# Optimization experiments

Measured on AMD Instinct MI355X. Metric: run time of the kernel, lower is better.

## Reference

```python
import jax, jax.numpy as jnp
import numpy as np


def _sine_theta(v1, v2):
    # v1, v2: [..., 2] edge direction vectors
    cross = v1[..., 0] * v2[..., 1] - v1[..., 1] * v2[..., 0]
    k = jnp.linalg.norm(v1, axis=-1) * jnp.linalg.norm(v2, axis=-1)
    return cross / k


def setup_inputs() -> dict:
    key = jax.random.key(0)
    P, N = 16384, 1024  # P polygons, N points each (N % 4 == 0)
    x_list = jax.random.normal(key, (P, N, 2), dtype=jnp.float32)
    return {"x_list": x_list, "scale": 1}


def reference(x_list, scale):
    # x_list: [P, N, 2] stacked polygons (equivalent to the original python list
    # when all polygons have the same point count N).
    P, N, _ = x_list.shape
    segn = N // 4
    # close the polygon and form consecutive edge vectors v[k] = x[k+1] - x[k]
    xc = jnp.concatenate([x_list, x_list[:, :1]], axis=1)  # [P, N+1, 2]
    v = xc[:, 1:] - xc[:, :-1]                             # [P, N, 2]
    idx = jnp.arange(segn) * 3
    v1 = v[:, idx]       # edge i*3
    v2 = v[:, idx + 1]   # edge i*3+1
    v3 = v[:, idx + 2]   # edge i*3+2
    s12 = _sine_theta(v1, v2)   # [P, segn]
    sina = _sine_theta(v1, v3)  # [P, segn]
    direct = (s12 >= 0).astype(x_list.dtype)
    term = direct * jax.nn.relu(-sina) + (1.0 - direct) * jax.nn.relu(sina)
    seg_loss = term.sum(axis=1) / segn  # [P]
    return (seg_loss * scale).mean()
```

## Files before the change

kernel.cpp:

```cpp
#include <hip/hip_runtime.h>


#define N_PTS     1024
#define SEGN      (N_PTS / 4)
#define BLOCK     256
#define ROW_F4    385

__global__ __launch_bounds__(BLOCK)
void xing_partial_kernel(const float* __restrict__ x,
                         float*       __restrict__ partial)
{
    const int p = blockIdx.x;
    const int t = threadIdx.x;

    __shared__ float rowf[ROW_F4 * 4];

    const float4* src = reinterpret_cast<const float4*>(x + (size_t)p * (N_PTS * 2));
    float4* dst = reinterpret_cast<float4*>(rowf);
    dst[t] = src[t];
    if (t < ROW_F4 - BLOCK) dst[BLOCK + t] = src[BLOCK + t];
    __syncthreads();

    const float2* pts = reinterpret_cast<const float2*>(rowf);
    const float2 a = pts[3 * t + 0];
    const float2 b = pts[3 * t + 1];
    const float2 c = pts[3 * t + 2];
    const float2 d = pts[3 * t + 3];

    const float v1x = b.x - a.x, v1y = b.y - a.y;
    const float v2x = c.x - b.x, v2y = c.y - b.y;
    const float v3x = d.x - c.x, v3y = d.y - c.y;

    const float cross12 = v1x * v2y - v1y * v2x;
    const float cross13 = v1x * v3y - v1y * v3x;

    const float n1 = v1x * v1x + v1y * v1y;
    const float n3 = v3x * v3x + v3y * v3y;
    const float sina = cross13 * rsqrtf(n1 * n3);

    float term = (cross12 >= 0.0f) ? fmaxf(-sina, 0.0f) : fmaxf(sina, 0.0f);

    #pragma unroll
    for (int off = 32; off > 0; off >>= 1)
        term += __shfl_down(term, off, 64);

    __shared__ float wsum[BLOCK / 64];
    const int lane = t & 63;
    const int wid  = t >> 6;
    if (lane == 0) wsum[wid] = term;
    __syncthreads();

    if (t == 0) {
        partial[p] = (wsum[0] + wsum[1]) + (wsum[2] + wsum[3]);
    }
}

__global__ __launch_bounds__(BLOCK)
void xing_reduce_kernel(const float* __restrict__ partial,
                        const int*   __restrict__ scale_p,
                        float*       __restrict__ out,
                        int P)
{
    const int t = threadIdx.x;
    const float4* pf4 = reinterpret_cast<const float4*>(partial);
    const int nf4 = P / 4;

    float sum = 0.0f;
    for (int i = t; i < nf4; i += BLOCK) {
        float4 v = pf4[i];
        sum += (v.x + v.y) + (v.z + v.w);
    }

    #pragma unroll
    for (int off = 32; off > 0; off >>= 1)
        sum += __shfl_down(sum, off, 64);

    __shared__ float wsum[BLOCK / 64];
    const int lane = t & 63;
    const int wid  = t >> 6;
    if (lane == 0) wsum[wid] = sum;
    __syncthreads();

    if (t == 0) {
        const float total = (wsum[0] + wsum[1]) + (wsum[2] + wsum[3]);
        out[0] = total * (float)(*scale_p) / ((float)SEGN * (float)P);
    }
}

extern "C" void kernel_launch(void* const* d_in, const int* in_sizes, int n_in,
                              void* d_out, int out_size, void* d_ws, size_t ws_size,
                              hipStream_t stream)
{
    const float* x       = (const float*)d_in[0];
    const int*   scale_p = (const int*)d_in[1];
    float*       out     = (float*)d_out;
    float*       partial = (float*)d_ws;

    const int P = in_sizes[0] / (N_PTS * 2);

    xing_partial_kernel<<<P, BLOCK, 0, stream>>>(x, partial);
    xing_reduce_kernel<<<1, BLOCK, 0, stream>>>(partial, scale_p, out, P);
}
```

Measured before the change: 182.5 us.

## Process eight polygons per block with double-buffered async global-to-LDS loads

Each block now handles eight polygons instead of one. It stages the next polygon's points straight into shared memory with the AMD global_load_lds builtin while computing on the current buffer, and accumulates per-thread terms across rows before a single block reduction. This is meant to hide load latency and cut per-block launch and reduction overhead. The trade-offs are fewer blocks, which means less memory-level parallelism across the grid, and reliance on the barrier correctly waiting for the async LDS loads to finish.

```diff
diff --git a/kernel.cpp b/kernel.cpp
--- a/kernel.cpp
+++ b/kernel.cpp
@@ -4,66 +4,88 @@
 #define N_PTS     1024
 #define SEGN      (N_PTS / 4)
 #define BLOCK     256
+#define ROWS      8
 #define ROW_F4    385
+#define ROW_FLT   (ROW_F4 * 4)
 
-__global__ __launch_bounds__(BLOCK)
+#define GLOAD_LDS16(g, l)                                                  \
+    __builtin_amdgcn_global_load_lds(                                      \
+        (const __attribute__((address_space(1))) unsigned int*)(g),        \
+        (__attribute__((address_space(3))) unsigned int*)(l), 16, 0, 0)
+
+__device__ __forceinline__ void stage_row(const float* __restrict__ rowsrc,
+                                          float* lbuf, int t)
+{
+    GLOAD_LDS16(rowsrc + 4 * t, lbuf + 4 * t);
+    if (t < ROW_F4 - BLOCK)
+        GLOAD_LDS16(rowsrc + 4 * (BLOCK + t), lbuf + 4 * (BLOCK + t));
+}
+
+__global__ __launch_bounds__(BLOCK, 8)
 void xing_partial_kernel(const float* __restrict__ x,
                          float*       __restrict__ partial)
 {
-    const int p = blockIdx.x;
     const int t = threadIdx.x;
+    const int b = blockIdx.x;
 
-    __shared__ float rowf[ROW_F4 * 4];
+    __shared__ float rowf[2][ROW_FLT];
 
-    const float4* src = reinterpret_cast<const float4*>(x + (size_t)p * (N_PTS * 2));
-    float4* dst = reinterpret_cast<float4*>(rowf);
-    dst[t] = src[t];
-    if (t < ROW_F4 - BLOCK) dst[BLOCK + t] = src[BLOCK + t];
-    __syncthreads();
+    const size_t row0 = (size_t)b * ROWS;
+    stage_row(x + row0 * (N_PTS * 2), rowf[0], t);
 
-    const float2* pts = reinterpret_cast<const float2*>(rowf);
-    const float2 a = pts[3 * t + 0];
-    const float2 b = pts[3 * t + 1];
-    const float2 c = pts[3 * t + 2];
-    const float2 d = pts[3 * t + 3];
+    float acc = 0.0f;
 
-    const float v1x = b.x - a.x, v1y = b.y - a.y;
-    const float v2x = c.x - b.x, v2y = c.y - b.y;
-    const float v3x = d.x - c.x, v3y = d.y - c.y;
+    #pragma unroll
+    for (int r = 0; r < ROWS; ++r) {
+        __syncthreads();
 
-    const float cross12 = v1x * v2y - v1y * v2x;
-    const float cross13 = v1x * v3y - v1y * v3x;
+        if (r + 1 < ROWS)
+            stage_row(x + (row0 + r + 1) * (size_t)(N_PTS * 2),
+                      rowf[(r + 1) & 1], t);
 
-    const float n1 = v1x * v1x + v1y * v1y;
-    const float n3 = v3x * v3x + v3y * v3y;
-    const float sina = cross13 * rsqrtf(n1 * n3);
+        const float2* pts = reinterpret_cast<const float2*>(rowf[r & 1]);
+        const float2 a = pts[3 * t + 0];
+        const float2 bb = pts[3 * t + 1];
+        const float2 c = pts[3 * t + 2];
+        const float2 d = pts[3 * t + 3];
 
-    float term = (cross12 >= 0.0f) ? fmaxf(-sina, 0.0f) : fmaxf(sina, 0.0f);
+        const float v1x = bb.x - a.x,  v1y = bb.y - a.y;
+        const float v2x = c.x - bb.x,  v2y = c.y - bb.y;
+        const float v3x = d.x - c.x,   v3y = d.y - c.y;
+
+        const float cross12 = v1x * v2y - v1y * v2x;
+        const float cross13 = v1x * v3y - v1y * v3x;
+
+        const float n1 = v1x * v1x + v1y * v1y;
+        const float n3 = v3x * v3x + v3y * v3y;
+        const float sina = cross13 * rsqrtf(n1 * n3);
+
+        acc += (cross12 >= 0.0f) ? fmaxf(-sina, 0.0f) : fmaxf(sina, 0.0f);
+    }
 
     #pragma unroll
     for (int off = 32; off > 0; off >>= 1)
-        term += __shfl_down(term, off, 64);
+        acc += __shfl_down(acc, off, 64);
 
     __shared__ float wsum[BLOCK / 64];
     const int lane = t & 63;
     const int wid  = t >> 6;
-    if (lane == 0) wsum[wid] = term;
+    if (lane == 0) wsum[wid] = acc;
     __syncthreads();
 
-    if (t == 0) {
-        partial[p] = (wsum[0] + wsum[1]) + (wsum[2] + wsum[3]);
-    }
+    if (t == 0)
+        partial[b] = (wsum[0] + wsum[1]) + (wsum[2] + wsum[3]);
 }
 
 __global__ __launch_bounds__(BLOCK)
 void xing_reduce_kernel(const float* __restrict__ partial,
                         const int*   __restrict__ scale_p,
                         float*       __restrict__ out,
-                        int P)
+                        int nblk, int P)
 {
     const int t = threadIdx.x;
     const float4* pf4 = reinterpret_cast<const float4*>(partial);
-    const int nf4 = P / 4;
+    const int nf4 = nblk / 4;
 
     float sum = 0.0f;
     for (int i = t; i < nf4; i += BLOCK) {
@@ -96,8 +118,9 @@
     float*       out     = (float*)d_out;
     float*       partial = (float*)d_ws;
 
-    const int P = in_sizes[0] / (N_PTS * 2);
+    const int P    = in_sizes[0] / (N_PTS * 2);
+    const int nblk = P / ROWS;
 
-    xing_partial_kernel<<<P, BLOCK, 0, stream>>>(x, partial);
-    xing_reduce_kernel<<<1, BLOCK, 0, stream>>>(partial, scale_p, out, P);
+    xing_partial_kernel<<<nblk, BLOCK, 0, stream>>>(x, partial);
+    xing_reduce_kernel<<<1, BLOCK, 0, stream>>>(partial, scale_p, out, nblk, P);
 }
```

Measured after the change: 184.6 us. Within noise of the previous version (+1.1%).

## Replace per-polygon blocks with grid-stride persistent loop over segments

Applied to the files above, without the earlier changes.

The partial kernel now launches a fixed grid of 2048 blocks that stride over all segments, reading points straight from global memory instead of staging each polygon row in shared memory. Each thread accumulates many segment terms before the wave reduction, so there are far fewer partial sums for the final kernel. This removes the per-block LDS copy and barrier and is meant to raise memory-level parallelism through the unrolled loop. The trade-off is uncached-looking strided float2 loads, which rely on cache for the overlapping neighbor points.

```diff
diff --git a/kernel.cpp b/kernel.cpp
--- a/kernel.cpp
+++ b/kernel.cpp
@@ -1,69 +1,72 @@
 #include <hip/hip_runtime.h>
 
 
-#define N_PTS     1024
-#define SEGN      (N_PTS / 4)
-#define BLOCK     256
-#define ROW_F4    385
+#define N_PTS 1024
+#define SEGN  (N_PTS / 4)
+#define BLOCK 256
+#define GRID  2048
 
 __global__ __launch_bounds__(BLOCK)
 void xing_partial_kernel(const float* __restrict__ x,
-                         float*       __restrict__ partial)
+                         float*       __restrict__ partial,
+                         int total_segs)
 {
-    const int p = blockIdx.x;
-    const int t = threadIdx.x;
+    const int t   = threadIdx.x;
+    const int tid = blockIdx.x * BLOCK + t;
+    const int gsz = gridDim.x * BLOCK;
 
-    __shared__ float rowf[ROW_F4 * 4];
+    const float2* __restrict__ pts = reinterpret_cast<const float2*>(x);
 
-    const float4* src = reinterpret_cast<const float4*>(x + (size_t)p * (N_PTS * 2));
-    float4* dst = reinterpret_cast<float4*>(rowf);
-    dst[t] = src[t];
-    if (t < ROW_F4 - BLOCK) dst[BLOCK + t] = src[BLOCK + t];
-    __syncthreads();
+    float acc = 0.0f;
 
-    const float2* pts = reinterpret_cast<const float2*>(rowf);
-    const float2 a = pts[3 * t + 0];
-    const float2 b = pts[3 * t + 1];
-    const float2 c = pts[3 * t + 2];
-    const float2 d = pts[3 * t + 3];
+    #pragma unroll 4
+    for (int g = tid; g < total_segs; g += gsz) {
+        const int p = g >> 8;
+        const int s = g & (SEGN - 1);
+        const float2* bp = pts + (p * (N_PTS) + 3 * s);
 
-    const float v1x = b.x - a.x, v1y = b.y - a.y;
-    const float v2x = c.x - b.x, v2y = c.y - b.y;
-    const float v3x = d.x - c.x, v3y = d.y - c.y;
+        const float2 a = bp[0];
+        const float2 b = bp[1];
+        const float2 c = bp[2];
+        const float2 d = bp[3];
 
-    const float cross12 = v1x * v2y - v1y * v2x;
-    const float cross13 = v1x * v3y - v1y * v3x;
+        const float v1x = b.x - a.x, v1y = b.y - a.y;
+        const float v2x = c.x - b.x, v2y = c.y - b.y;
+        const float v3x = d.x - c.x, v3y = d.y - c.y;
 
-    const float n1 = v1x * v1x + v1y * v1y;
-    const float n3 = v3x * v3x + v3y * v3y;
-    const float sina = cross13 * rsqrtf(n1 * n3);
+        const float cross12 = v1x * v2y - v1y * v2x;
+        const float cross13 = v1x * v3y - v1y * v3x;
 
-    float term = (cross12 >= 0.0f) ? fmaxf(-sina, 0.0f) : fmaxf(sina, 0.0f);
+        const float n1 = v1x * v1x + v1y * v1y;
+        const float n3 = v3x * v3x + v3y * v3y;
+        const float sina = cross13 * rsqrtf(n1 * n3);
+
+        acc += (cross12 >= 0.0f) ? fmaxf(-sina, 0.0f) : fmaxf(sina, 0.0f);
+    }
 
     #pragma unroll
     for (int off = 32; off > 0; off >>= 1)
-        term += __shfl_down(term, off, 64);
+        acc += __shfl_down(acc, off, 64);
 
     __shared__ float wsum[BLOCK / 64];
     const int lane = t & 63;
     const int wid  = t >> 6;
-    if (lane == 0) wsum[wid] = term;
+    if (lane == 0) wsum[wid] = acc;
     __syncthreads();
 
-    if (t == 0) {
-        partial[p] = (wsum[0] + wsum[1]) + (wsum[2] + wsum[3]);
-    }
+    if (t == 0)
+        partial[blockIdx.x] = (wsum[0] + wsum[1]) + (wsum[2] + wsum[3]);
 }
 
 __global__ __launch_bounds__(BLOCK)
 void xing_reduce_kernel(const float* __restrict__ partial,
                         const int*   __restrict__ scale_p,
                         float*       __restrict__ out,
-                        int P)
+                        int nblk, int P)
 {
     const int t = threadIdx.x;
     const float4* pf4 = reinterpret_cast<const float4*>(partial);
-    const int nf4 = P / 4;
+    const int nf4 = nblk / 4;
 
     float sum = 0.0f;
     for (int i = t; i < nf4; i += BLOCK) {
@@ -97,7 +100,8 @@
     float*       partial = (float*)d_ws;
 
     const int P = in_sizes[0] / (N_PTS * 2);
+    const int total_segs = P * SEGN;
 
-    xing_partial_kernel<<<P, BLOCK, 0, stream>>>(x, partial);
-    xing_reduce_kernel<<<1, BLOCK, 0, stream>>>(partial, scale_p, out, P);
+    xing_partial_kernel<<<GRID, BLOCK, 0, stream>>>(x, partial, total_segs);
+    xing_reduce_kernel<<<1, BLOCK, 0, stream>>>(partial, scale_p, out, GRID, P);
 }
```

Result: no change. 185.4 us (+1.6%).
